# Kernel tuning notes

Measured on AMD Instinct MI355X. Metric: run time of the kernel, lower is better.

The kernel has to match this reference:

```python
import jax, jax.numpy as jnp
import numpy as np


def setup_inputs() -> dict:
    key = jax.random.key(0)
    k1, k2, k3 = jax.random.split(key, 3)
    B, C, H, W = 8, 256, 64, 64
    l = jax.random.normal(k1, (B, C, H, W), dtype=jnp.float32)
    # 1x1 conv weights [out=C//2, in=C]; scale 1/sqrt(C) so projected features have ~unit variance
    scale = 1.0 / np.sqrt(C)
    w_theta = jax.random.normal(k2, (C // 2, C), dtype=jnp.float32) * scale
    w_phi = jax.random.normal(k3, (C // 2, C), dtype=jnp.float32) * scale
    return {"l": l, "w_theta": w_theta, "w_phi": w_phi}


def reference(l, w_theta, w_phi):
    # NonLocalOp forward with embed=True, softmax=True
    B, C, H, W = l.shape
    E = w_theta.shape[0]  # C // 2
    HW = H * W
    # 1x1 convs == per-pixel linear maps
    theta = jnp.einsum('bchw,ec->behw', l, w_theta).reshape(B, E, HW)  # [B,E,HW]
    phi = jnp.einsum('bchw,ec->behw', l, w_phi).reshape(B, E, HW)      # [B,E,HW]
    g = l.reshape(B, C, HW)                                            # [B,C,HW]
    # scores: theta^T phi over embed channels, scaled by sqrt(C//2)
    scale = 1.0 / jnp.sqrt(jnp.asarray(C // 2, dtype=l.dtype))
    f = jnp.einsum('beq,bek->bqk', theta, phi) * scale                 # [B,HW,HW]
    f = jax.nn.softmax(f, axis=-1)
    out = jnp.einsum('bqk,bck->bcq', f, g).reshape(B, C, H, W)
    return out
```

## Files before the change

kernel.cpp:

```cpp
#include <hip/hip_runtime.h>
#include <stdint.h>

#define NB 8
#define NC 256
#define NE 128
#define NHW 4096

typedef __bf16 v8bf __attribute__((ext_vector_type(8)));
typedef float v4f __attribute__((ext_vector_type(4)));
typedef float v16f __attribute__((ext_vector_type(16)));
typedef unsigned int v4u __attribute__((ext_vector_type(4)));
typedef unsigned int v2u __attribute__((ext_vector_type(2)));

typedef unsigned int __attribute__((address_space(1))) uint_g;
typedef unsigned int __attribute__((address_space(3))) uint_l;

#if __has_builtin(__builtin_amdgcn_exp2f)
#define EXP2F(x) __builtin_amdgcn_exp2f(x)
#else
#define EXP2F(x) exp2f(x)
#endif

#define BARRIER_LDS() asm volatile("s_waitcnt lgkmcnt(0)\n\ts_barrier" ::: "memory")
#define WAIT_VM0()    asm volatile("s_waitcnt vmcnt(0)" ::: "memory")

__device__ __forceinline__ void dma16(const unsigned short* g, unsigned short* l) {
    __builtin_amdgcn_global_load_lds((const uint_g*)g, (uint_l*)l, 16, 0, 0);
}

__device__ __forceinline__ unsigned short f2bf(float x) {
    union { float f; unsigned int u; } v; v.f = x;
    unsigned int r = v.u + 0x7fffu + ((v.u >> 16) & 1u);
    return (unsigned short)(r >> 16);
}

__device__ __forceinline__ unsigned int pack_bf2_ru(float a, float b) {
    union { float f; unsigned int u; } va, vb; va.f = a; vb.f = b;
    return ((va.u + 0x8000u) >> 16) | ((vb.u + 0x8000u) & 0xffff0000u);
}

__global__ __launch_bounds__(256) void cast_w_kernel(const float* __restrict__ wt,
                                                     const float* __restrict__ wp,
                                                     unsigned short* __restrict__ Wbf) {
    int i = blockIdx.x * 256 + threadIdx.x;
    const float QS = 0.08838834764831845f * 1.4426950408889634f;
    float v = (i < 32768) ? wt[i] * QS : wp[i - 32768];
    Wbf[i] = f2bf(v);
}

__global__ __launch_bounds__(256, 2) void proj_kernel(const float* __restrict__ l,
                                                      const unsigned short* __restrict__ Wbf,
                                                      unsigned short* __restrict__ Qbf,
                                                      unsigned short* __restrict__ Kbf,
                                                      unsigned short* __restrict__ Vbf) {
    __shared__ __align__(16) unsigned short A[64][264];
    __shared__ __align__(16) unsigned short Ost[2][32][136];
    const int tid = threadIdx.x;
    const int b = blockIdx.x & 7;
    const int qt = (blockIdx.x >> 3) << 6;
    const float* lb = l + ((size_t)b * NC * NHW + qt);

    for (int s = 0; s < 16; ++s) {
        int f = tid + s * 256;
        int c = f >> 4, j = f & 15;
        float4 v = *(const float4*)(lb + (size_t)c * NHW + j * 4);
        ushort4 o4;
        o4.x = f2bf(v.x); o4.y = f2bf(v.y); o4.z = f2bf(v.z); o4.w = f2bf(v.w);
        A[j * 4 + 0][c] = o4.x;
        A[j * 4 + 1][c] = o4.y;
        A[j * 4 + 2][c] = o4.z;
        A[j * 4 + 3][c] = o4.w;
        unsigned int d0 = (unsigned int)o4.x | ((unsigned int)o4.y << 16);
        unsigned int d1 = (unsigned int)o4.z | ((unsigned int)o4.w << 16);
        unsigned int p0 = (unsigned int)__shfl_xor((int)d0, 1);
        unsigned int p1 = (unsigned int)__shfl_xor((int)d1, 1);
        if ((j & 1) == 0) {
            *(v4u*)(Vbf + (size_t)b * 1048576 +
                    ((size_t)((qt >> 3) + (j >> 1)) * 256 + c) * 8) = (v4u){d0, d1, p0, p1};
        }
    }
    __syncthreads();

    const int w = tid >> 6, L = tid & 63;
    const int l15 = L & 15, q4 = L >> 4;
    const v4f vz = {0.f, 0.f, 0.f, 0.f};
    v4f acc[4][4];
    for (int mt = 0; mt < 4; ++mt)
        for (int nt = 0; nt < 4; ++nt) acc[mt][nt] = vz;

    for (int kf = 0; kf < 8; ++kf) {
        int kc = kf * 32 + q4 * 8;
        v8bf a[4], bb[4];
        for (int mt = 0; mt < 4; ++mt)
            a[mt] = *(const v8bf*)&A[mt * 16 + l15][kc];
        for (int nt = 0; nt < 4; ++nt)
            bb[nt] = *(const v8bf*)(Wbf + (w * 64 + nt * 16 + l15) * 256 + kc);
        for (int mt = 0; mt < 4; ++mt)
            for (int nt = 0; nt < 4; ++nt)
                acc[mt][nt] = __builtin_amdgcn_mfma_f32_16x16x32_bf16(a[mt], bb[nt], acc[mt][nt], 0, 0, 0);
    }

    const int side = w >> 1;
    const int ebase = (w & 1) * 64;
#pragma unroll
    for (int ph = 0; ph < 2; ++ph) {
        __syncthreads();
#pragma unroll
        for (int mh = 0; mh < 2; ++mh) {
            int mt = ph * 2 + mh;
#pragma unroll
            for (int nt = 0; nt < 4; ++nt)
#pragma unroll
                for (int r = 0; r < 4; ++r) {
                    int q32 = mh * 16 + q4 * 4 + r;
                    Ost[side][q32][ebase + nt * 16 + l15] = f2bf(acc[mt][nt][r]);
                }
        }
        __syncthreads();
#pragma unroll
        for (int s = 0; s < 4; ++s) {
            int idx = tid + s * 256;
            int sd = idx >> 9, rem = idx & 511;
            int r32 = rem >> 4, c8 = rem & 15;
            unsigned short* dst = sd ? Kbf : Qbf;
            int c8s = sd ? (c8 ^ (r32 & 15)) : c8;
            *(uint4*)(dst + ((size_t)b * NHW + qt + ph * 32 + r32) * NE + c8s * 8) =
                *(const uint4*)&Ost[sd][r32][c8 * 8];
        }
    }
}

__global__ __launch_bounds__(512, 2) void attn_kernel(const unsigned short* __restrict__ Qbf,
                                                      const unsigned short* __restrict__ Kbf,
                                                      const unsigned short* __restrict__ Vbf,
                                                      float* __restrict__ out) {
    __shared__ __align__(16) unsigned char smem[131584];
    unsigned short* KuS = (unsigned short*)smem;
    unsigned short* PuS = (unsigned short*)(smem + 65536);
    float* lsumF = (float*)(smem + 131072);

    const int tid = threadIdx.x;
    const int b = blockIdx.x & 7;
    const int q128 = (blockIdx.x >> 3) << 7;
    const int w = tid >> 6;
    const int L = tid & 63;
    const int l31 = L & 31, hi = L >> 5;
    const int x15 = l31 & 15;

    const unsigned short* Kb = Kbf + (size_t)b * NHW * NE;
    const unsigned short* Vt = Vbf + (size_t)b * 1048576;

    if (w < 4) {
        float lacc = 0.f;
        v8bf bq[8];
        const unsigned short* qrow = Qbf + ((size_t)b * NHW + q128 + w * 32 + l31) * NE + hi * 8;
#pragma unroll
        for (int ef = 0; ef < 8; ++ef)
            bq[ef] = *(const v8bf*)(qrow + ef * 16);
#pragma unroll
        for (int jj = 0; jj < 8; ++jj) {
            int j = w * 8 + jj;
            dma16(Kb + (size_t)j * 512 + L * 8, KuS + j * 512);
        }
        WAIT_VM0();
        BARRIER_LDS();
#pragma unroll
        for (int jj = 0; jj < 8; ++jj) {
            int j = w * 8 + jj;
            dma16(Kb + (size_t)16384 + j * 512 + L * 8, KuS + 16384 + j * 512);
        }
        v16f s_prev[4];
        {
            v16f tmp[4];
#pragma unroll
            for (int kt = 0; kt < 4; ++kt)
#pragma unroll
                for (int r = 0; r < 16; ++r) { s_prev[kt][r] = 0.f; tmp[kt][r] = 0.f; }
#pragma unroll
            for (int ef = 0; ef < 4; ++ef)
#pragma unroll
                for (int kt = 0; kt < 4; ++kt) {
                    const unsigned short* krow = KuS + (kt * 32 + l31) * 128;
                    v8bf ak0 = *(const v8bf*)(krow + (((2 * ef + hi) ^ x15) * 8));
                    v8bf ak1 = *(const v8bf*)(krow + (((2 * (ef + 4) + hi) ^ x15) * 8));
                    s_prev[kt] = __builtin_amdgcn_mfma_f32_32x32x16_bf16(ak0, bq[ef], s_prev[kt], 0, 0, 0);
                    tmp[kt]    = __builtin_amdgcn_mfma_f32_32x32x16_bf16(ak1, bq[ef + 4], tmp[kt], 0, 0, 0);
                }
#pragma unroll
            for (int kt = 0; kt < 4; ++kt)
#pragma unroll
                for (int r = 0; r < 16; ++r) s_prev[kt][r] += tmp[kt][r];
        }
        WAIT_VM0();
        BARRIER_LDS();

        const int a1 = l31 * 8 + hi * 4;
        const int a2 = (l31 + 32) * 8 + hi * 4;

        for (int it = 0; it < 33; ++it) {
            if (it < 32) {
                const int buf = it & 1;
                if (it <= 29) {
                    const size_t kro = (size_t)(it + 2) * 16384;
#pragma unroll
                    for (int jj = 0; jj < 8; ++jj) {
                        int j = w * 8 + jj;
                        dma16(Kb + kro + j * 512 + L * 8, KuS + buf * 16384 + j * 512);
                    }
                }
#pragma unroll
                for (int kt = 0; kt < 4; ++kt) {
                    float p[16];
#pragma unroll
                    for (int r = 0; r < 16; ++r) p[r] = EXP2F(s_prev[kt][r]);
                    {
                        float t0 = (p[0] + p[1]) + (p[2] + p[3]);
                        float t1 = (p[4] + p[5]) + (p[6] + p[7]);
                        float t2 = (p[8] + p[9]) + (p[10] + p[11]);
                        float t3 = (p[12] + p[13]) + (p[14] + p[15]);
                        lacc += (t0 + t1) + (t2 + t3);
                    }
                    unsigned int pk[8];
#pragma unroll
                    for (int t = 0; t < 8; ++t) pk[t] = pack_bf2_ru(p[2 * t], p[2 * t + 1]);
                    unsigned short* base0 = PuS + buf * 16384 + (w * 8 + kt * 2) * 512;
                    *(v2u*)(base0 + a1)       = (v2u){pk[0], pk[1]};
                    *(v2u*)(base0 + a2)       = (v2u){pk[2], pk[3]};
                    *(v2u*)(base0 + 512 + a1) = (v2u){pk[4], pk[5]};
                    *(v2u*)(base0 + 512 + a2) = (v2u){pk[6], pk[7]};
                }
                if (it <= 30) {
                    const unsigned short* kub = KuS + ((it + 1) & 1) * 16384;
                    v16f tmp[4];
#pragma unroll
                    for (int kt = 0; kt < 4; ++kt)
#pragma unroll
                        for (int r = 0; r < 16; ++r) { s_prev[kt][r] = 0.f; tmp[kt][r] = 0.f; }
#pragma unroll
                    for (int ef = 0; ef < 4; ++ef)
#pragma unroll
                        for (int kt = 0; kt < 4; ++kt) {
                            const unsigned short* krow = kub + (kt * 32 + l31) * 128;
                            v8bf ak0 = *(const v8bf*)(krow + (((2 * ef + hi) ^ x15) * 8));
                            v8bf ak1 = *(const v8bf*)(krow + (((2 * (ef + 4) + hi) ^ x15) * 8));
                            s_prev[kt] = __builtin_amdgcn_mfma_f32_32x32x16_bf16(ak0, bq[ef], s_prev[kt], 0, 0, 0);
                            tmp[kt]    = __builtin_amdgcn_mfma_f32_32x32x16_bf16(ak1, bq[ef + 4], tmp[kt], 0, 0, 0);
                        }
#pragma unroll
                    for (int kt = 0; kt < 4; ++kt)
#pragma unroll
                        for (int r = 0; r < 16; ++r) s_prev[kt][r] += tmp[kt][r];
                }
                WAIT_VM0();
            }
            BARRIER_LDS();
        }
        float tot = lacc + __shfl_xor(lacc, 32);
        if (hi == 0) lsumF[w * 32 + l31] = tot;
        BARRIER_LDS();
    } else {
        const int ci = w - 4;
        v16f o[2][4];
#pragma unroll
        for (int ct = 0; ct < 2; ++ct)
#pragma unroll
            for (int qt = 0; qt < 4; ++qt)
#pragma unroll
                for (int r = 0; r < 16; ++r) o[ct][qt][r] = 0.f;
        const int crow0 = ci * 64 + l31;
        const int crow1 = ci * 64 + 32 + l31;
        v8bf av[2][4];
#pragma unroll
        for (int kf = 0; kf < 4; ++kf) {
            av[0][kf] = *(const v8bf*)(Vt + ((size_t)((kf * 2 + hi) * 256) + crow0) * 8);
            av[1][kf] = *(const v8bf*)(Vt + ((size_t)((kf * 2 + hi) * 256) + crow1) * 8);
        }
        BARRIER_LDS();
        BARRIER_LDS();

        for (int it = 0; it < 33; ++it) {
            if (it > 0) {
                const size_t uA = (size_t)(it - 1) * 16;
                v8bf av2[2][4];
#pragma unroll
                for (int kf = 0; kf < 4; ++kf) {
                    av2[0][kf] = *(const v8bf*)(Vt + ((uA + (kf + 4) * 2 + hi) * 256 + crow0) * 8);
                    av2[1][kf] = *(const v8bf*)(Vt + ((uA + (kf + 4) * 2 + hi) * 256 + crow1) * 8);
                }
                const int pbuf = (it - 1) & 1;
                const unsigned short* pb = PuS + pbuf * 16384 + (hi * 32 + l31) * 8;
#pragma unroll
                for (int kf = 0; kf < 4; ++kf) {
                    v8bf bp[4];
#pragma unroll
                    for (int qt = 0; qt < 4; ++qt)
                        bp[qt] = *(const v8bf*)(pb + (qt * 8 + kf) * 512);
#pragma unroll
                    for (int qt = 0; qt < 4; ++qt) {
                        o[0][qt] = __builtin_amdgcn_mfma_f32_32x32x16_bf16(av[0][kf], bp[qt], o[0][qt], 0, 0, 0);
                        o[1][qt] = __builtin_amdgcn_mfma_f32_32x32x16_bf16(av[1][kf], bp[qt], o[1][qt], 0, 0, 0);
                    }
                }
#pragma unroll
                for (int kf = 0; kf < 4; ++kf) {
                    v8bf bp[4];
#pragma unroll
                    for (int qt = 0; qt < 4; ++qt)
                        bp[qt] = *(const v8bf*)(pb + (qt * 8 + 4 + kf) * 512);
#pragma unroll
                    for (int qt = 0; qt < 4; ++qt) {
                        o[0][qt] = __builtin_amdgcn_mfma_f32_32x32x16_bf16(av2[0][kf], bp[qt], o[0][qt], 0, 0, 0);
                        o[1][qt] = __builtin_amdgcn_mfma_f32_32x32x16_bf16(av2[1][kf], bp[qt], o[1][qt], 0, 0, 0);
                    }
                }
                const size_t uB = (size_t)(it & 31) * 16;
#pragma unroll
                for (int kf = 0; kf < 4; ++kf) {
                    av[0][kf] = *(const v8bf*)(Vt + ((uB + kf * 2 + hi) * 256 + crow0) * 8);
                    av[1][kf] = *(const v8bf*)(Vt + ((uB + kf * 2 + hi) * 256 + crow1) * 8);
                }
            }
            BARRIER_LDS();
        }
        BARRIER_LDS();
        float inv[4];
#pragma unroll
        for (int qt = 0; qt < 4; ++qt) inv[qt] = 1.0f / lsumF[qt * 32 + l31];
#pragma unroll
        for (int ct = 0; ct < 2; ++ct)
#pragma unroll
            for (int qt = 0; qt < 4; ++qt) {
                float* ob = out + (size_t)b * NC * NHW + q128 + qt * 32 + l31;
#pragma unroll
                for (int r = 0; r < 16; ++r) {
                    int c = ci * 64 + ct * 32 + (r & 3) + 8 * (r >> 2) + 4 * hi;
                    ob[(size_t)c * NHW] = o[ct][qt][r] * inv[qt];
                }
            }
    }
}

extern "C" void kernel_launch(void* const* d_in, const int* in_sizes, int n_in,
                              void* d_out, int out_size, void* d_ws, size_t ws_size,
                              hipStream_t stream) {
    const float* l  = (const float*)d_in[0];
    const float* wt = (const float*)d_in[1];
    const float* wp = (const float*)d_in[2];
    float* out = (float*)d_out;

    char* ws = (char*)d_ws;
    unsigned short* Wbf = (unsigned short*)ws;
    unsigned short* Qbf = (unsigned short*)(ws + 131072);
    unsigned short* Kbf = (unsigned short*)(ws + 131072 + 8388608);
    unsigned short* Vbf = (unsigned short*)(ws + 131072 + 16777216);

    hipLaunchKernelGGL(cast_w_kernel, dim3(256), dim3(256), 0, stream, wt, wp, Wbf);
    hipLaunchKernelGGL(proj_kernel,   dim3(512), dim3(256), 0, stream, l, Wbf, Qbf, Kbf, Vbf);
    hipLaunchKernelGGL(attn_kernel,   dim3(256), dim3(512), 0, stream, Qbf, Kbf, Vbf, out);
}
```

Before: 197.2 us.

## Halve attention tiles to 64 queries and 64 keys with 256-thread blocks

The attention kernel moves from 128-query blocks of 512 threads to 64-query blocks of 256 threads. Each block runs 2 score/softmax waves and 2 PV waves, and each PV wave now covers 128 channels instead of 64. Key tiles shrink from 128 to 64 keys, so the loop runs 64 iterations instead of 32. LDS per block drops from about 128 KB to about 48 KB, and the grid doubles to 512 blocks, which may let more blocks share a CU. In exchange, each V element is reused by fewer queries, so V is read from memory twice as often, and there are twice as many barrier-synchronised iterations.

Measured after the change: 209.3 us. 1.06x slower.

```diff
diff --git a/kernel.cpp b/kernel.cpp
--- a/kernel.cpp
+++ b/kernel.cpp
@@ -130,18 +130,18 @@
     }
 }
 
-__global__ __launch_bounds__(512, 2) void attn_kernel(const unsigned short* __restrict__ Qbf,
+__global__ __launch_bounds__(256, 2) void attn_kernel(const unsigned short* __restrict__ Qbf,
                                                       const unsigned short* __restrict__ Kbf,
                                                       const unsigned short* __restrict__ Vbf,
                                                       float* __restrict__ out) {
-    __shared__ __align__(16) unsigned char smem[131584];
+    __shared__ __align__(16) unsigned char smem[49408];
     unsigned short* KuS = (unsigned short*)smem;
-    unsigned short* PuS = (unsigned short*)(smem + 65536);
-    float* lsumF = (float*)(smem + 131072);
+    unsigned short* PuS = (unsigned short*)(smem + 32768);
+    float* lsumF = (float*)(smem + 49152);
 
     const int tid = threadIdx.x;
     const int b = blockIdx.x & 7;
-    const int q128 = (blockIdx.x >> 3) << 7;
+    const int q64 = (blockIdx.x >> 3) << 6;
     const int w = tid >> 6;
     const int L = tid & 63;
     const int l31 = L & 31, hi = L >> 5;
@@ -150,10 +150,10 @@
     const unsigned short* Kb = Kbf + (size_t)b * NHW * NE;
     const unsigned short* Vt = Vbf + (size_t)b * 1048576;
 
-    if (w < 4) {
+    if (w < 2) {
         float lacc = 0.f;
         v8bf bq[8];
-        const unsigned short* qrow = Qbf + ((size_t)b * NHW + q128 + w * 32 + l31) * NE + hi * 8;
+        const unsigned short* qrow = Qbf + ((size_t)b * NHW + q64 + w * 32 + l31) * NE + hi * 8;
 #pragma unroll
         for (int ef = 0; ef < 8; ++ef)
             bq[ef] = *(const v8bf*)(qrow + ef * 16);
@@ -167,19 +167,19 @@
 #pragma unroll
         for (int jj = 0; jj < 8; ++jj) {
             int j = w * 8 + jj;
-            dma16(Kb + (size_t)16384 + j * 512 + L * 8, KuS + 16384 + j * 512);
-        }
-        v16f s_prev[4];
+            dma16(Kb + (size_t)8192 + j * 512 + L * 8, KuS + 8192 + j * 512);
+        }
+        v16f s_prev[2];
         {
-            v16f tmp[4];
-#pragma unroll
-            for (int kt = 0; kt < 4; ++kt)
+            v16f tmp[2];
+#pragma unroll
+            for (int kt = 0; kt < 2; ++kt)
 #pragma unroll
                 for (int r = 0; r < 16; ++r) { s_prev[kt][r] = 0.f; tmp[kt][r] = 0.f; }
 #pragma unroll
             for (int ef = 0; ef < 4; ++ef)
 #pragma unroll
-                for (int kt = 0; kt < 4; ++kt) {
+                for (int kt = 0; kt < 2; ++kt) {
                     const unsigned short* krow = KuS + (kt * 32 + l31) * 128;
                     v8bf ak0 = *(const v8bf*)(krow + (((2 * ef + hi) ^ x15) * 8));
                     v8bf ak1 = *(const v8bf*)(krow + (((2 * (ef + 4) + hi) ^ x15) * 8));
@@ -187,7 +187,7 @@
                     tmp[kt]    = __builtin_amdgcn_mfma_f32_32x32x16_bf16(ak1, bq[ef + 4], tmp[kt], 0, 0, 0);
                 }
 #pragma unroll
-            for (int kt = 0; kt < 4; ++kt)
+            for (int kt = 0; kt < 2; ++kt)
 #pragma unroll
                 for (int r = 0; r < 16; ++r) s_prev[kt][r] += tmp[kt][r];
         }
@@ -197,19 +197,19 @@
         const int a1 = l31 * 8 + hi * 4;
         const int a2 = (l31 + 32) * 8 + hi * 4;
 
-        for (int it = 0; it < 33; ++it) {
-            if (it < 32) {
+        for (int it = 0; it < 65; ++it) {
+            if (it < 64) {
                 const int buf = it & 1;
-                if (it <= 29) {
-                    const size_t kro = (size_t)(it + 2) * 16384;
+                if (it <= 61) {
+                    const size_t kro = (size_t)(it + 2) * 8192;
 #pragma unroll
                     for (int jj = 0; jj < 8; ++jj) {
                         int j = w * 8 + jj;
-                        dma16(Kb + kro + j * 512 + L * 8, KuS + buf * 16384 + j * 512);
+                        dma16(Kb + kro + j * 512 + L * 8, KuS + buf * 8192 + j * 512);
                     }
                 }
 #pragma unroll
-                for (int kt = 0; kt < 4; ++kt) {
+                for (int kt = 0; kt < 2; ++kt) {
                     float p[16];
 #pragma unroll
                     for (int r = 0; r < 16; ++r) p[r] = EXP2F(s_prev[kt][r]);
@@ -223,23 +223,23 @@
                     unsigned int pk[8];
 #pragma unroll
                     for (int t = 0; t < 8; ++t) pk[t] = pack_bf2_ru(p[2 * t], p[2 * t + 1]);
-                    unsigned short* base0 = PuS + buf * 16384 + (w * 8 + kt * 2) * 512;
+                    unsigned short* base0 = PuS + buf * 4096 + (w * 4 + kt * 2) * 512;
                     *(v2u*)(base0 + a1)       = (v2u){pk[0], pk[1]};
                     *(v2u*)(base0 + a2)       = (v2u){pk[2], pk[3]};
                     *(v2u*)(base0 + 512 + a1) = (v2u){pk[4], pk[5]};
                     *(v2u*)(base0 + 512 + a2) = (v2u){pk[6], pk[7]};
                 }
-                if (it <= 30) {
-                    const unsigned short* kub = KuS + ((it + 1) & 1) * 16384;
-                    v16f tmp[4];
-#pragma unroll
-                    for (int kt = 0; kt < 4; ++kt)
+                if (it <= 62) {
+                    const unsigned short* kub = KuS + ((it + 1) & 1) * 8192;
+                    v16f tmp[2];
+#pragma unroll
+                    for (int kt = 0; kt < 2; ++kt)
 #pragma unroll
                         for (int r = 0; r < 16; ++r) { s_prev[kt][r] = 0.f; tmp[kt][r] = 0.f; }
 #pragma unroll
                     for (int ef = 0; ef < 4; ++ef)
 #pragma unroll
-                        for (int kt = 0; kt < 4; ++kt) {
+                        for (int kt = 0; kt < 2; ++kt) {
                             const unsigned short* krow = kub + (kt * 32 + l31) * 128;
                             v8bf ak0 = *(const v8bf*)(krow + (((2 * ef + hi) ^ x15) * 8));
                             v8bf ak1 = *(const v8bf*)(krow + (((2 * (ef + 4) + hi) ^ x15) * 8));
@@ -247,7 +247,7 @@
                             tmp[kt]    = __builtin_amdgcn_mfma_f32_32x32x16_bf16(ak1, bq[ef + 4], tmp[kt], 0, 0, 0);
                         }
 #pragma unroll
-                    for (int kt = 0; kt < 4; ++kt)
+                    for (int kt = 0; kt < 2; ++kt)
 #pragma unroll
                         for (int r = 0; r < 16; ++r) s_prev[kt][r] += tmp[kt][r];
                 }
@@ -259,81 +259,63 @@
         if (hi == 0) lsumF[w * 32 + l31] = tot;
         BARRIER_LDS();
     } else {
-        const int ci = w - 4;
-        v16f o[2][4];
-#pragma unroll
-        for (int ct = 0; ct < 2; ++ct)
-#pragma unroll
-            for (int qt = 0; qt < 4; ++qt)
+        const int ci = w - 2;
+        v16f o[4][2];
+#pragma unroll
+        for (int ct = 0; ct < 4; ++ct)
+#pragma unroll
+            for (int qt = 0; qt < 2; ++qt)
 #pragma unroll
                 for (int r = 0; r < 16; ++r) o[ct][qt][r] = 0.f;
-        const int crow0 = ci * 64 + l31;
-        const int crow1 = ci * 64 + 32 + l31;
-        v8bf av[2][4];
-#pragma unroll
-        for (int kf = 0; kf < 4; ++kf) {
-            av[0][kf] = *(const v8bf*)(Vt + ((size_t)((kf * 2 + hi) * 256) + crow0) * 8);
-            av[1][kf] = *(const v8bf*)(Vt + ((size_t)((kf * 2 + hi) * 256) + crow1) * 8);
-        }
-        BARRIER_LDS();
-        BARRIER_LDS();
-
-        for (int it = 0; it < 33; ++it) {
+        int crow[4];
+#pragma unroll
+        for (int ct = 0; ct < 4; ++ct) crow[ct] = ci * 128 + ct * 32 + l31;
+        v8bf av[4][4];
+#pragma unroll
+        for (int ct = 0; ct < 4; ++ct)
+#pragma unroll
+            for (int kf = 0; kf < 4; ++kf)
+                av[ct][kf] = *(const v8bf*)(Vt + ((size_t)((kf * 2 + hi) * 256) + crow[ct]) * 8);
+        BARRIER_LDS();
+        BARRIER_LDS();
+
+        for (int it = 0; it < 65; ++it) {
             if (it > 0) {
-                const size_t uA = (size_t)(it - 1) * 16;
-                v8bf av2[2][4];
+                const int pbuf = (it - 1) & 1;
+                const unsigned short* pb = PuS + pbuf * 4096 + (hi * 32 + l31) * 8;
 #pragma unroll
                 for (int kf = 0; kf < 4; ++kf) {
-                    av2[0][kf] = *(const v8bf*)(Vt + ((uA + (kf + 4) * 2 + hi) * 256 + crow0) * 8);
-                    av2[1][kf] = *(const v8bf*)(Vt + ((uA + (kf + 4) * 2 + hi) * 256 + crow1) * 8);
-                }
-                const int pbuf = (it - 1) & 1;
-                const unsigned short* pb = PuS + pbuf * 16384 + (hi * 32 + l31) * 8;
-#pragma unroll
-                for (int kf = 0; kf < 4; ++kf) {
-                    v8bf bp[4];
-#pragma unroll
-                    for (int qt = 0; qt < 4; ++qt)
-                        bp[qt] = *(const v8bf*)(pb + (qt * 8 + kf) * 512);
-#pragma unroll
-                    for (int qt = 0; qt < 4; ++qt) {
-                        o[0][qt] = __builtin_amdgcn_mfma_f32_32x32x16_bf16(av[0][kf], bp[qt], o[0][qt], 0, 0, 0);
-                        o[1][qt] = __builtin_amdgcn_mfma_f32_32x32x16_bf16(av[1][kf], bp[qt], o[1][qt], 0, 0, 0);
-                    }
-                }
-#pragma unroll
-                for (int kf = 0; kf < 4; ++kf) {
-                    v8bf bp[4];
-#pragma unroll
-                    for (int qt = 0; qt < 4; ++qt)
-                        bp[qt] = *(const v8bf*)(pb + (qt * 8 + 4 + kf) * 512);
-#pragma unroll
-                    for (int qt = 0; qt < 4; ++qt) {
-                        o[0][qt] = __builtin_amdgcn_mfma_f32_32x32x16_bf16(av2[0][kf], bp[qt], o[0][qt], 0, 0, 0);
-                        o[1][qt] = __builtin_amdgcn_mfma_f32_32x32x16_bf16(av2[1][kf], bp[qt], o[1][qt], 0, 0, 0);
-                    }
-                }
-                const size_t uB = (size_t)(it & 31) * 16;
-#pragma unroll
-                for (int kf = 0; kf < 4; ++kf) {
-                    av[0][kf] = *(const v8bf*)(Vt + ((uB + kf * 2 + hi) * 256 + crow0) * 8);
-                    av[1][kf] = *(const v8bf*)(Vt + ((uB + kf * 2 + hi) * 256 + crow1) * 8);
-                }
+                    v8bf bp[2];
+#pragma unroll
+                    for (int qt = 0; qt < 2; ++qt)
+                        bp[qt] = *(const v8bf*)(pb + (qt * 4 + kf) * 512);
+#pragma unroll
+                    for (int ct = 0; ct < 4; ++ct)
+#pragma unroll
+                        for (int qt = 0; qt < 2; ++qt)
+                            o[ct][qt] = __builtin_amdgcn_mfma_f32_32x32x16_bf16(av[ct][kf], bp[qt], o[ct][qt], 0, 0, 0);
+                }
+                const size_t uB = (size_t)(it & 63) * 8;
+#pragma unroll
+                for (int ct = 0; ct < 4; ++ct)
+#pragma unroll
+                    for (int kf = 0; kf < 4; ++kf)
+                        av[ct][kf] = *(const v8bf*)(Vt + ((uB + kf * 2 + hi) * 256 + crow[ct]) * 8);
             }
             BARRIER_LDS();
         }
         BARRIER_LDS();
-        float inv[4];
-#pragma unroll
-        for (int qt = 0; qt < 4; ++qt) inv[qt] = 1.0f / lsumF[qt * 32 + l31];
-#pragma unroll
-        for (int ct = 0; ct < 2; ++ct)
-#pragma unroll
-            for (int qt = 0; qt < 4; ++qt) {
-                float* ob = out + (size_t)b * NC * NHW + q128 + qt * 32 + l31;
+        float inv[2];
+#pragma unroll
+        for (int qt = 0; qt < 2; ++qt) inv[qt] = 1.0f / lsumF[qt * 32 + l31];
+#pragma unroll
+        for (int ct = 0; ct < 4; ++ct)
+#pragma unroll
+            for (int qt = 0; qt < 2; ++qt) {
+                float* ob = out + (size_t)b * NC * NHW + q64 + qt * 32 + l31;
 #pragma unroll
                 for (int r = 0; r < 16; ++r) {
-                    int c = ci * 64 + ct * 32 + (r & 3) + 8 * (r >> 2) + 4 * hi;
+                    int c = ci * 128 + ct * 32 + (r & 3) + 8 * (r >> 2) + 4 * hi;
                     ob[(size_t)c * NHW] = o[ct][qt][r] * inv[qt];
                 }
             }
@@ -356,5 +338,5 @@
 
     hipLaunchKernelGGL(cast_w_kernel, dim3(256), dim3(256), 0, stream, wt, wp, Wbf);
     hipLaunchKernelGGL(proj_kernel,   dim3(512), dim3(256), 0, stream, l, Wbf, Qbf, Kbf, Vbf);
-    hipLaunchKernelGGL(attn_kernel,   dim3(256), dim3(512), 0, stream, Qbf, Kbf, Vbf, out);
-}
+    hipLaunchKernelGGL(attn_kernel,   dim3(512), dim3(256), 0, stream, Qbf, Kbf, Vbf, out);
+}
```
